# Optimization experiments

Hardware: AMD Instinct MI355X
Metric: run time of the kernel (lower is better)

Reference implementation:

```python
import jax, jax.numpy as jnp
import numpy as np
from jax import lax

SAMPLE_RATE = 0.25
RADIUS = 0.5
NSAMPLE = 32
MLP = [64 + 3, 64, 128]  # use_xyz adds 3 to first width


def setup_inputs() -> dict:
    key = jax.random.key(0)
    ks = jax.random.split(key, 8)
    B, N, C = 8, 8192, 64
    pos = jax.random.normal(ks[0], (B, N, 3), dtype=jnp.float32)
    features = jax.random.normal(ks[1], (B, C, N), dtype=jnp.float32)
    # shared MLP (1x1 Conv2d with bias, ReLU), He-scaled init
    w0 = jax.random.normal(ks[2], (MLP[1], MLP[0]), jnp.float32) * (2.0 / MLP[0]) ** 0.5
    b0 = jnp.zeros((MLP[1],), jnp.float32)
    w1 = jax.random.normal(ks[3], (MLP[1], MLP[1]), jnp.float32) * (2.0 / MLP[1]) ** 0.5
    b1 = jnp.zeros((MLP[1],), jnp.float32)
    w2 = jax.random.normal(ks[4], (MLP[2], MLP[1]), jnp.float32) * (2.0 / MLP[1]) ** 0.5
    b2 = jnp.zeros((MLP[2],), jnp.float32)
    return {"pos": pos, "features": features, "w0": w0, "b0": b0,
            "w1": w1, "b1": b1, "w2": w2, "b2": b2}


def furthest_point_sample(pos, npoint):
    """pos: (B,N,3) -> idx (B,npoint) int32, greedy FPS starting at index 0."""
    B, N, _ = pos.shape
    init_idx = jnp.zeros((B,), jnp.int32)
    init_d = jnp.full((B, N), 1e10, jnp.float32)

    def step(carry, _):
        dists, last = carry
        p_last = jnp.take_along_axis(pos, last[:, None, None], axis=1)  # (B,1,3)
        d = jnp.sum((pos - p_last) ** 2, axis=-1)                        # (B,N)
        dists = jnp.minimum(dists, d)
        nxt = jnp.argmax(dists, axis=-1).astype(jnp.int32)
        return (dists, nxt), nxt

    (_, _), rest = lax.scan(step, (init_d, init_idx), None, length=npoint - 1)
    return jnp.concatenate([init_idx[None, :], rest], axis=0).T  # (B,npoint)


def ball_query(pos, new_xyz, nsample, radius):
    """pos (B,N,3), new_xyz (B,S,3) -> idx (B,S,nsample): first nsample pts
    within radius, padded with the first hit (0 if no hit), as in PointNet2 CUDA."""
    B, N, _ = pos.shape
    d2 = jnp.sum((new_xyz[:, :, None, :] - pos[:, None, :, :]) ** 2, axis=-1)  # (B,S,N)
    cand = jnp.where(d2 < radius * radius,
                     jnp.arange(N, dtype=jnp.int32)[None, None, :], N)
    neg_top, _ = lax.top_k(-cand, nsample)     # smallest nsample indices
    idx = -neg_top                              # ascending index order
    first = idx[..., :1]
    pad = jnp.where(first == N, 0, first)
    return jnp.where(idx == N, pad, idx)


def reference(pos, features, w0, b0, w1, b1, w2, b2):
    B, N, _ = pos.shape
    npoint = int(N * SAMPLE_RATE)
    fps_idx = furthest_point_sample(pos, npoint)                         # (B,S)
    new_xyz = jax.vmap(lambda p, i: p[i])(pos, fps_idx)                  # (B,S,3)

    idx = ball_query(pos, new_xyz, NSAMPLE, RADIUS)                      # (B,S,K)
    grouped_xyz = jax.vmap(lambda p, i: p[i])(pos, idx)                  # (B,S,K,3)
    rel_xyz = grouped_xyz - new_xyz[:, :, None, :]                       # (B,S,K,3)
    grouped_feat = jax.vmap(lambda f, i: f[:, i])(features, idx)         # (B,C,S,K)
    x = jnp.concatenate([rel_xyz.transpose(0, 3, 1, 2), grouped_feat], axis=1)  # (B,3+C,S,K)

    def conv_relu(x, w, b):  # 1x1 conv + bias + ReLU
        y = jnp.einsum('oc,bcsk->bosk', w, x) + b[None, :, None, None]
        return jax.nn.relu(y)

    x = conv_relu(x, w0, b0)
    x = conv_relu(x, w1, b1)
    x = conv_relu(x, w2, b2)
    new_features = jnp.max(x, axis=-1)                                   # (B,mlp[-1],S)
    return new_xyz, new_features
```

## Files before the change

kernel.cpp:

```cpp
#include <hip/hip_runtime.h>

#define NB 8
#define NPTS 8192
#define NC_FEAT 64
#define NS 2048
#define NK 32

typedef float v2f __attribute__((ext_vector_type(2)));

__device__ __forceinline__ float d2_ref(float px, float py, float pz,
                                        float qx, float qy, float qz) {
  float dx = __fsub_rn(px, qx);
  float dy = __fsub_rn(py, qy);
  float dz = __fsub_rn(pz, qz);
  return __fadd_rn(__fadd_rn(__fmul_rn(dx, dx), __fmul_rn(dy, dy)),
                   __fmul_rn(dz, dz));
}

#define DPP_KEYMAX(key, ctrl)                                                 \
  {                                                                           \
    unsigned _lo = (unsigned)__builtin_amdgcn_update_dpp(                     \
        0, (int)(unsigned)(key), (ctrl), 0xf, 0xf, true);                     \
    unsigned _hi = (unsigned)__builtin_amdgcn_update_dpp(                     \
        0, (int)(unsigned)((key) >> 32), (ctrl), 0xf, 0xf, true);             \
    unsigned long long _o = ((unsigned long long)_hi << 32) | _lo;            \
    if (_o > (key)) (key) = _o;                                               \
  }

__global__ __launch_bounds__(256)
void k_fps(const float* __restrict__ pos, float* __restrict__ new_xyz) {
#pragma clang fp contract(off)
  __shared__ __align__(16) float smem[3 * NPTS + 16];
  float* sx = smem;
  float* sy = smem + NPTS;
  float* sz = smem + 2 * NPTS;
  unsigned long long* rk = (unsigned long long*)(smem + 3 * NPTS);

  const int tid = threadIdx.x;
  const int b = blockIdx.x;
  const float* p = pos + (size_t)b * NPTS * 3;

  for (int i = tid; i < NPTS; i += 256) {
    sx[i] = p[3 * i + 0];
    sy[i] = p[3 * i + 1];
    sz[i] = p[3 * i + 2];
  }
  if (tid < 8) rk[tid] = 0ull;
  __syncthreads();

  const int base = tid * 32;
  v2f px[16], py[16], pz[16], di[16];
#pragma unroll
  for (int k = 0; k < 16; ++k) {
    px[k] = *(const v2f*)&sx[base + 2 * k];
    py[k] = *(const v2f*)&sy[base + 2 * k];
    pz[k] = *(const v2f*)&sz[base + 2 * k];
    di[k] = (v2f){1e10f, 1e10f};
  }
  if (tid == 0) {
    new_xyz[((size_t)b * NS) * 3 + 0] = sx[0];
    new_xyz[((size_t)b * NS) * 3 + 1] = sy[0];
    new_xyz[((size_t)b * NS) * 3 + 2] = sz[0];
  }

  const int lane = tid & 63;
  const int wave = tid >> 6;
  int last = 0, buf = 0;

  for (int it = 1; it < NS; ++it) {
    float qx = sx[last], qy = sy[last], qz = sz[last];
    v2f nqx = (v2f){-qx, -qx};
    v2f nqy = (v2f){-qy, -qy};
    v2f nqz = (v2f){-qz, -qz};
    float bd = -1.0f;
    int bj = 0;
#pragma unroll
    for (int k = 0; k < 16; ++k) {
      v2f t0, t1, t2, d2v;
      asm("v_pk_add_f32 %0, %4, %7\n\t"
          "v_pk_add_f32 %1, %5, %8\n\t"
          "v_pk_add_f32 %2, %6, %9\n\t"
          "v_pk_mul_f32 %0, %0, %0\n\t"
          "v_pk_mul_f32 %1, %1, %1\n\t"
          "v_pk_mul_f32 %2, %2, %2\n\t"
          "v_pk_add_f32 %3, %0, %1\n\t"
          "v_pk_add_f32 %3, %3, %2"
          : "=&v"(t0), "=&v"(t1), "=&v"(t2), "=&v"(d2v)
          : "v"(px[k]), "v"(py[k]), "v"(pz[k]), "v"(nqx), "v"(nqy), "v"(nqz));
      di[k] = __builtin_elementwise_min(di[k], d2v);
      if (di[k].x > bd) { bd = di[k].x; bj = 2 * k; }
      if (di[k].y > bd) { bd = di[k].y; bj = 2 * k + 1; }
    }
    unsigned long long key =
        ((unsigned long long)__float_as_uint(bd) << 32) |
        (unsigned)~(unsigned)(base + bj);
    DPP_KEYMAX(key, 0x111);
    DPP_KEYMAX(key, 0x112);
    DPP_KEYMAX(key, 0x114);
    DPP_KEYMAX(key, 0x118);
    DPP_KEYMAX(key, 0x142);
    DPP_KEYMAX(key, 0x143);
    if (lane == 63) rk[buf * 4 + wave] = key;
    __syncthreads();
    key = rk[buf * 4 + (lane & 3)];
    DPP_KEYMAX(key, 0x111);
    DPP_KEYMAX(key, 0x112);
    int fi = (int)~(unsigned)__builtin_amdgcn_readlane((int)(unsigned)key, 3);
    last = fi;
    buf ^= 1;
    if (tid == 0) {
      new_xyz[((size_t)b * NS + it) * 3 + 0] = sx[fi];
      new_xyz[((size_t)b * NS + it) * 3 + 1] = sy[fi];
      new_xyz[((size_t)b * NS + it) * 3 + 2] = sz[fi];
    }
  }
}

__global__ __launch_bounds__(256)
void k_tp(const float* __restrict__ feat, const float* __restrict__ w0,
          const float* __restrict__ w1, const float* __restrict__ w2,
          float* __restrict__ featT, float* __restrict__ wT) {
  __shared__ float tile[64 * 65];
  const int tid = threadIdx.x;
  if (blockIdx.x < NB * (NPTS / 64)) {
    const int t = blockIdx.x;
    const int b = t >> 7;
    const int n0 = (t & 127) << 6;
    const int col = tid & 63;
    const int r0 = tid >> 6;
#pragma unroll
    for (int q = 0; q < 16; ++q) {
      int c = r0 + q * 4;
      tile[c * 65 + col] = feat[((size_t)b * NC_FEAT + c) * NPTS + n0 + col];
    }
    __syncthreads();
#pragma unroll
    for (int q = 0; q < 16; ++q) {
      int r = r0 + q * 4;
      featT[((size_t)b * NPTS + n0 + r) * 64 + col] = tile[col * 65 + r];
    }
  } else {
    for (int i = tid; i < 67 * 64; i += 256)
      wT[i] = w0[(i & 63) * 67 + (i >> 6)];
    for (int i = tid; i < 64 * 64; i += 256)
      wT[67 * 64 + i] = w1[(i & 63) * 64 + (i >> 6)];
    for (int i = tid; i < 64 * 128; i += 256)
      wT[67 * 64 + 64 * 64 + i] = w2[(i & 127) * 64 + (i >> 7)];
  }
}

__global__ __launch_bounds__(256)
void k_ball(const float* __restrict__ pos, const float* __restrict__ nxyz,
            int* __restrict__ ballidx) {
  const int wid = (blockIdx.x * 256 + threadIdx.x) >> 6;
  const int lane = threadIdx.x & 63;
  const int b = wid >> 11;
  const float qx = nxyz[wid * 3 + 0];
  const float qy = nxyz[wid * 3 + 1];
  const float qz = nxyz[wid * 3 + 2];
  const float* p = pos + (size_t)b * NPTS * 3;
  int* outp = ballidx + (size_t)wid * NK;

  int cnt = 0;
  int firstidx = 0x7fffffff;
  for (int n0 = 0; n0 < NPTS; n0 += 64) {
    const int i = n0 + lane;
    float d2 = d2_ref(p[3 * i], p[3 * i + 1], p[3 * i + 2], qx, qy, qz);
    bool hit = d2 < 0.25f;
    unsigned long long mask = __ballot(hit);
    int pre = __popcll(mask & ((1ull << lane) - 1ull));
    int slot = cnt + pre;
    if (hit && slot < NK) outp[slot] = i;
    if (hit && slot == 0) firstidx = i;
    cnt += __popcll(mask);
    if (cnt >= NK) break;
  }
#pragma unroll
  for (int m = 32; m >= 1; m >>= 1)
    firstidx = min(firstidx, __shfl_xor(firstidx, m, 64));
  int pad = (firstidx == 0x7fffffff) ? 0 : firstidx;
  int start = cnt < NK ? cnt : NK;
  if (lane < NK && lane >= start) outp[lane] = pad;
}

#define MLP_FMA16(wr, xc, acc)                                   \
  _Pragma("unroll") for (int o4 = 0; o4 < 16; ++o4) {            \
    float4 w = (wr)[o4];                                         \
    (acc)[o4 * 4 + 0] = fmaf(w.x, (xc), (acc)[o4 * 4 + 0]);      \
    (acc)[o4 * 4 + 1] = fmaf(w.y, (xc), (acc)[o4 * 4 + 1]);      \
    (acc)[o4 * 4 + 2] = fmaf(w.z, (xc), (acc)[o4 * 4 + 2]);      \
    (acc)[o4 * 4 + 3] = fmaf(w.w, (xc), (acc)[o4 * 4 + 3]);      \
  }

__global__ __launch_bounds__(256)
void k_mlp(const float* __restrict__ pos, const float* __restrict__ featT,
           const float* __restrict__ wT, const float* __restrict__ b0,
           const float* __restrict__ b1, const float* __restrict__ b2,
           const int* __restrict__ ballidx, const float* __restrict__ nxyz,
           float* __restrict__ outf) {
  __shared__ float xs[64 * 256];
  const int tid = threadIdx.x;
  const int g = blockIdx.x * 256 + tid;
  const int s = (g >> 5) & (NS - 1);
  const int b = g >> 16;

  const int idx = ballidx[g];
  const float qx = nxyz[((size_t)b * NS + s) * 3 + 0];
  const float qy = nxyz[((size_t)b * NS + s) * 3 + 1];
  const float qz = nxyz[((size_t)b * NS + s) * 3 + 2];
  const float* pp = pos + ((size_t)b * NPTS + idx) * 3;
  const float x0 = __fsub_rn(pp[0], qx);
  const float x1 = __fsub_rn(pp[1], qy);
  const float x2 = __fsub_rn(pp[2], qz);

  const float4* fT = (const float4*)(featT + ((size_t)b * NPTS + idx) * 64);
#pragma unroll
  for (int c4 = 0; c4 < 16; ++c4) {
    float4 v = fT[c4];
    xs[(c4 * 4 + 0) * 256 + tid] = v.x;
    xs[(c4 * 4 + 1) * 256 + tid] = v.y;
    xs[(c4 * 4 + 2) * 256 + tid] = v.z;
    xs[(c4 * 4 + 3) * 256 + tid] = v.w;
  }

  const float* wt0 = wT;
  const float* wt1 = wT + 67 * 64;
  const float* wt2 = wT + 67 * 64 + 64 * 64;

  float acc[64];
#pragma unroll
  for (int o = 0; o < 64; ++o) acc[o] = b0[o];
  {
    const float xr0 = x0, xr1 = x1, xr2 = x2;
    const float4* wr;
    wr = (const float4*)(wt0 + 0 * 64); MLP_FMA16(wr, xr0, acc);
    wr = (const float4*)(wt0 + 1 * 64); MLP_FMA16(wr, xr1, acc);
    wr = (const float4*)(wt0 + 2 * 64); MLP_FMA16(wr, xr2, acc);
  }
  for (int c = 0; c < 64; ++c) {
    float xc = xs[c * 256 + tid];
    const float4* wr = (const float4*)(wt0 + (3 + c) * 64);
    MLP_FMA16(wr, xc, acc);
  }
#pragma unroll
  for (int o = 0; o < 64; ++o) xs[o * 256 + tid] = fmaxf(acc[o], 0.0f);

#pragma unroll
  for (int o = 0; o < 64; ++o) acc[o] = b1[o];
  for (int c = 0; c < 64; ++c) {
    float xc = xs[c * 256 + tid];
    const float4* wr = (const float4*)(wt1 + c * 64);
    MLP_FMA16(wr, xc, acc);
  }
#pragma unroll
  for (int o = 0; o < 64; ++o) xs[o * 256 + tid] = fmaxf(acc[o], 0.0f);

#pragma unroll
  for (int h = 0; h < 2; ++h) {
#pragma unroll
    for (int o = 0; o < 64; ++o) acc[o] = b2[h * 64 + o];
    for (int c = 0; c < 64; ++c) {
      float xc = xs[c * 256 + tid];
      const float4* wr = (const float4*)(wt2 + c * 128 + h * 64);
      MLP_FMA16(wr, xc, acc);
    }
#pragma unroll
    for (int o = 0; o < 64; ++o) {
      float v = fmaxf(acc[o], 0.0f);
      v = fmaxf(v, __shfl_xor(v, 16, 64));
      v = fmaxf(v, __shfl_xor(v, 8, 64));
      v = fmaxf(v, __shfl_xor(v, 4, 64));
      v = fmaxf(v, __shfl_xor(v, 2, 64));
      v = fmaxf(v, __shfl_xor(v, 1, 64));
      if ((tid & 31) == 0)
        outf[((size_t)b * 128 + h * 64 + o) * NS + s] = v;
    }
  }
}

extern "C" void kernel_launch(void* const* d_in, const int* in_sizes, int n_in,
                              void* d_out, int out_size, void* d_ws,
                              size_t ws_size, hipStream_t stream) {
  const float* pos = (const float*)d_in[0];
  const float* feat = (const float*)d_in[1];
  const float* w0 = (const float*)d_in[2];
  const float* b0 = (const float*)d_in[3];
  const float* w1 = (const float*)d_in[4];
  const float* b1 = (const float*)d_in[5];
  const float* w2 = (const float*)d_in[6];
  const float* b2 = (const float*)d_in[7];

  float* out = (float*)d_out;
  float* new_xyz = out;
  float* new_feat = out + (size_t)NB * NS * 3;

  int* ballidx = (int*)d_ws;
  float* featT = (float*)d_ws + (size_t)NB * NS * NK;
  float* wT = featT + (size_t)NB * NPTS * 64;

  hipLaunchKernelGGL(k_tp, dim3(NB * (NPTS / 64) + 1), dim3(256), 0, stream,
                     feat, w0, w1, w2, featT, wT);
  hipLaunchKernelGGL(k_fps, dim3(NB), dim3(256), 0, stream, pos, new_xyz);
  hipLaunchKernelGGL(k_ball, dim3((NB * NS) / 4), dim3(256), 0, stream, pos,
                     new_xyz, ballidx);
  hipLaunchKernelGGL(k_mlp, dim3((NB * NS * NK) / 256), dim3(256), 0, stream,
                     pos, featT, wT, b0, b1, b2, ballidx, new_xyz, new_feat);
}
```

Measured before the change: 2.524 ms.

## Split furthest point sampling across eight cooperating blocks per batch with global-memory sync

FPS now runs eight blocks per batch instead of one, each owning 1024 points. Per-iteration argmax keys go to a double-buffered global slot array, and every wave spins on atomic loads until all 32 wave slots carry the current iteration tag. This spreads the serial FPS loop's per-iteration arithmetic over more CUs. In exchange it adds a cross-block spin barrier through L2 on every iteration and assumes all 64 blocks are co-resident. Slots are never reset, so the iteration tag in the key is what tells fresh entries from stale ones.

New measurement: 5.642 ms. 2.24x slower.

```diff
diff --git a/kernel.cpp b/kernel.cpp
--- a/kernel.cpp
+++ b/kernel.cpp
@@ -26,47 +26,51 @@
     unsigned long long _o = ((unsigned long long)_hi << 32) | _lo;            \
     if (_o > (key)) (key) = _o;                                               \
   }
+#define DPP_KEYMAX6(key)                                                      \
+  DPP_KEYMAX(key, 0x111); DPP_KEYMAX(key, 0x112); DPP_KEYMAX(key, 0x114);     \
+  DPP_KEYMAX(key, 0x118); DPP_KEYMAX(key, 0x142); DPP_KEYMAX(key, 0x143)
 
 __global__ __launch_bounds__(256)
-void k_fps(const float* __restrict__ pos, float* __restrict__ new_xyz) {
+void k_fps(const float* __restrict__ pos, float* __restrict__ new_xyz,
+           unsigned long long* __restrict__ slots) {
 #pragma clang fp contract(off)
-  __shared__ __align__(16) float smem[3 * NPTS + 16];
+  __shared__ __align__(16) float smem[3 * NPTS];
   float* sx = smem;
   float* sy = smem + NPTS;
   float* sz = smem + 2 * NPTS;
-  unsigned long long* rk = (unsigned long long*)(smem + 3 * NPTS);
 
   const int tid = threadIdx.x;
-  const int b = blockIdx.x;
+  const int b = blockIdx.x >> 3;
+  const int blk = blockIdx.x & 7;
+  const int lane = tid & 63;
+  const int wave = tid >> 6;
+  const int wid = blk * 4 + wave;
   const float* p = pos + (size_t)b * NPTS * 3;
+  unsigned long long* sb = slots + (size_t)b * 64;
 
   for (int i = tid; i < NPTS; i += 256) {
     sx[i] = p[3 * i + 0];
     sy[i] = p[3 * i + 1];
     sz[i] = p[3 * i + 2];
   }
-  if (tid < 8) rk[tid] = 0ull;
   __syncthreads();
 
-  const int base = tid * 32;
-  v2f px[16], py[16], pz[16], di[16];
-#pragma unroll
-  for (int k = 0; k < 16; ++k) {
+  const int base = blk * 1024 + tid * 4;
+  v2f px[2], py[2], pz[2], di[2];
+#pragma unroll
+  for (int k = 0; k < 2; ++k) {
     px[k] = *(const v2f*)&sx[base + 2 * k];
     py[k] = *(const v2f*)&sy[base + 2 * k];
     pz[k] = *(const v2f*)&sz[base + 2 * k];
     di[k] = (v2f){1e10f, 1e10f};
   }
-  if (tid == 0) {
+  if (blk == 0 && tid == 0) {
     new_xyz[((size_t)b * NS) * 3 + 0] = sx[0];
     new_xyz[((size_t)b * NS) * 3 + 1] = sy[0];
     new_xyz[((size_t)b * NS) * 3 + 2] = sz[0];
   }
 
-  const int lane = tid & 63;
-  const int wave = tid >> 6;
-  int last = 0, buf = 0;
-
+  int last = 0;
   for (int it = 1; it < NS; ++it) {
     float qx = sx[last], qy = sy[last], qz = sz[last];
     v2f nqx = (v2f){-qx, -qx};
@@ -75,7 +79,7 @@
     float bd = -1.0f;
     int bj = 0;
 #pragma unroll
-    for (int k = 0; k < 16; ++k) {
+    for (int k = 0; k < 2; ++k) {
       v2f t0, t1, t2, d2v;
       asm("v_pk_add_f32 %0, %4, %7\n\t"
           "v_pk_add_f32 %1, %5, %8\n\t"
@@ -93,22 +97,24 @@
     }
     unsigned long long key =
         ((unsigned long long)__float_as_uint(bd) << 32) |
-        (unsigned)~(unsigned)(base + bj);
-    DPP_KEYMAX(key, 0x111);
-    DPP_KEYMAX(key, 0x112);
-    DPP_KEYMAX(key, 0x114);
-    DPP_KEYMAX(key, 0x118);
-    DPP_KEYMAX(key, 0x142);
-    DPP_KEYMAX(key, 0x143);
-    if (lane == 63) rk[buf * 4 + wave] = key;
-    __syncthreads();
-    key = rk[buf * 4 + (lane & 3)];
-    DPP_KEYMAX(key, 0x111);
-    DPP_KEYMAX(key, 0x112);
-    int fi = (int)~(unsigned)__builtin_amdgcn_readlane((int)(unsigned)key, 3);
+        ((unsigned long long)(unsigned)(it & 0x7FF) << 13) |
+        (unsigned long long)(unsigned)(8191 - (base + bj));
+    DPP_KEYMAX6(key);
+    unsigned long long* pbuf = sb + (it & 1) * 32;
+    if (lane == 63)
+      __hip_atomic_store(&pbuf[wid], key, __ATOMIC_RELAXED,
+                         __HIP_MEMORY_SCOPE_AGENT);
+    unsigned long long k2;
+    const unsigned tgt = (unsigned)(it & 0x7FF);
+    do {
+      k2 = __hip_atomic_load(&pbuf[lane & 31], __ATOMIC_RELAXED,
+                             __HIP_MEMORY_SCOPE_AGENT);
+    } while (!__all((((unsigned)(k2 >> 13)) & 0x7FFu) == tgt));
+    DPP_KEYMAX6(k2);
+    int low = __builtin_amdgcn_readlane((int)(unsigned)k2, 63);
+    int fi = 8191 - (int)((unsigned)low & 0x1FFFu);
     last = fi;
-    buf ^= 1;
-    if (tid == 0) {
+    if (blk == 0 && tid == 0) {
       new_xyz[((size_t)b * NS + it) * 3 + 0] = sx[fi];
       new_xyz[((size_t)b * NS + it) * 3 + 1] = sy[fi];
       new_xyz[((size_t)b * NS + it) * 3 + 2] = sz[fi];
@@ -294,13 +300,15 @@
   float* new_xyz = out;
   float* new_feat = out + (size_t)NB * NS * 3;
 
-  int* ballidx = (int*)d_ws;
-  float* featT = (float*)d_ws + (size_t)NB * NS * NK;
+  unsigned long long* slots = (unsigned long long*)d_ws;
+  int* ballidx = (int*)((char*)d_ws + 4096);
+  float* featT = (float*)((char*)d_ws + 4096 + (size_t)NB * NS * NK * 4);
   float* wT = featT + (size_t)NB * NPTS * 64;
 
   hipLaunchKernelGGL(k_tp, dim3(NB * (NPTS / 64) + 1), dim3(256), 0, stream,
                      feat, w0, w1, w2, featT, wT);
-  hipLaunchKernelGGL(k_fps, dim3(NB), dim3(256), 0, stream, pos, new_xyz);
+  hipLaunchKernelGGL(k_fps, dim3(NB * 8), dim3(256), 0, stream, pos, new_xyz,
+                     slots);
   hipLaunchKernelGGL(k_ball, dim3((NB * NS) / 4), dim3(256), 0, stream, pos,
                      new_xyz, ballidx);
   hipLaunchKernelGGL(k_mlp, dim3((NB * NS * NK) / 256), dim3(256), 0, stream,
```
